# Kernel optimization log

Hardware: AMD Instinct MI355X
Metric: run time of the kernel (lower is better)

The kernel has to match this reference:

```python
import jax, jax.numpy as jnp
import numpy as np

B, T_D, T_P = 64, 256, 1024
DRUG_DIM, PROT_DIM, D = 128, 128, 128
MAX_LEN = 1024
NEG = -1e9


def _linear_params(k, out_d, in_d):
    k1, k2 = jax.random.split(k)
    lim = 1.0 / np.sqrt(in_d)
    W = jax.random.uniform(k1, (out_d, in_d), minval=-lim, maxval=lim, dtype=jnp.float32)
    b = jax.random.uniform(k2, (out_d,), minval=-lim, maxval=lim, dtype=jnp.float32)
    return W, b


def setup_inputs() -> dict:
    key = jax.random.key(0)
    ks = jax.random.split(key, 13)
    inp = {
        'smiles_embeddings': jax.random.normal(ks[0], (B, T_D, DRUG_DIM), dtype=jnp.float32),
        'protein_embeddings': jax.random.normal(ks[1], (B, T_P, PROT_DIM), dtype=jnp.float32),
        'smiles_mask': jax.random.randint(ks[2], (B, T_D), 0, 2, dtype=jnp.int32),
        'protein_mask': jax.random.randint(ks[3], (B, T_P), 0, 2, dtype=jnp.int32),
        # torch inits pos_bias to zeros; small random values make the test nontrivial
        'pos_bias': 0.02 * jax.random.normal(ks[4], (MAX_LEN, MAX_LEN), dtype=jnp.float32),
    }
    names = [('Wqd', 'bqd', DRUG_DIM), ('Wkp', 'bkp', PROT_DIM), ('Wvp', 'bvp', PROT_DIM),
             ('Wqp', 'bqp', PROT_DIM), ('Wkd', 'bkd', DRUG_DIM), ('Wvd', 'bvd', DRUG_DIM),
             ('Wpd', 'bpd', D), ('Wpp', 'bpp', D)]
    for i, (wn, bn, in_d) in enumerate(names):
        W, b = _linear_params(ks[5 + i], D, in_d)
        inp[wn] = W
        inp[bn] = b
    return inp


def _lin(x, W, b):
    return x @ W.T + b


def _aft(q, k, v, pb_masked, Wp, bp):
    # q: [B,Ti,D]; k,v: [B,Tj,D]; pb_masked: [B,Ti,Tj]
    max_k = k.max(axis=1, keepdims=True)              # per (b,d) over seq j
    max_pb = pb_masked.max(axis=2, keepdims=True)     # per (b,i) over j
    exp_k = jnp.exp(k - max_k)                        # [B,Tj,D]
    exp_pb = jnp.exp(pb_masked - max_pb)              # [B,Ti,Tj]
    num = jnp.einsum('bij,bjd->bid', exp_pb, exp_k * v)
    den = jnp.einsum('bij,bjd->bid', exp_pb, exp_k)
    y = jax.nn.sigmoid(q) * num / den
    return _lin(y, Wp, bp)


def reference(smiles_embeddings, protein_embeddings, smiles_mask, protein_mask, pos_bias,
              Wqd, bqd, Wkp, bkp, Wvp, bvp, Wqp, bqp, Wkd, bkd, Wvd, bvd, Wpd, bpd, Wpp, bpp):
    Td = smiles_embeddings.shape[1]
    Tp = protein_embeddings.shape[1]
    combined = smiles_mask[:, :, None] * protein_mask[:, None, :]  # [B,Td,Tp]
    pb = pos_bias[:Td, :Tp][None]                                   # [1,Td,Tp]

    # drug queries attend over protein keys/values
    pb_d = jnp.where(combined == 0, NEG, pb)
    y_d = _aft(_lin(smiles_embeddings, Wqd, bqd),
               _lin(protein_embeddings, Wkp, bkp),
               _lin(protein_embeddings, Wvp, bvp), pb_d, Wpd, bpd)

    # protein queries attend over drug keys/values (transposed pos bias)
    pb_p = jnp.where(jnp.swapaxes(combined, 1, 2) == 0, NEG, jnp.swapaxes(pb, 1, 2))
    y_p = _aft(_lin(protein_embeddings, Wqp, bqp),
               _lin(smiles_embeddings, Wkd, bkd),
               _lin(smiles_embeddings, Wvd, bvd), pb_p, Wpp, bpp)

    y_d = jnp.where(smiles_mask[:, :, None] == 0, NEG, y_d).max(axis=1)   # [B,D]
    y_p = jnp.where(protein_mask[:, :, None] == 0, NEG, y_p).max(axis=1)  # [B,D]
    return y_d, y_p
```

## Files before the change

### kernel.cpp

```cpp
#include <hip/hip_runtime.h>
#include <cstdint>
#include <cstddef>

#define NEGV -1e9f

typedef __bf16 bf16x8 __attribute__((ext_vector_type(8)));
typedef float f32x4 __attribute__((ext_vector_type(4)));
typedef unsigned short us4 __attribute__((ext_vector_type(4)));
typedef unsigned short us8 __attribute__((ext_vector_type(8)));

__device__ __forceinline__ unsigned short f2bf(float f) {
  unsigned int u = __float_as_uint(f);
  u += 0x7fffu + ((u >> 16) & 1u);
  return (unsigned short)(u >> 16);
}
__device__ __forceinline__ float bf2f(unsigned short u) {
  return __uint_as_float(((unsigned)u) << 16);
}

__device__ __forceinline__ void gld16(const void* g, void* l) {
  __builtin_amdgcn_global_load_lds(
      (const __attribute__((address_space(1))) unsigned int*)g,
      (__attribute__((address_space(3))) unsigned int*)l, 16, 0, 0);
}

__global__ void wcvt_kernel(const float* __restrict__ w0, const float* __restrict__ w1,
                            const float* __restrict__ w2, const float* __restrict__ w3,
                            const float* __restrict__ w4, const float* __restrict__ w5,
                            const float* __restrict__ w6, const float* __restrict__ w7,
                            unsigned short* __restrict__ dst) {
  const float* Ws[8] = {w0, w1, w2, w3, w4, w5, w6, w7};
  const float* src = Ws[blockIdx.y];
  int idx = blockIdx.x * 256 + threadIdx.x;
  float4 v = *(const float4*)&src[(size_t)idx * 4];
  us4 p;
  p.x = f2bf(v.x); p.y = f2bf(v.y); p.z = f2bf(v.z); p.w = f2bf(v.w);
  *(us4*)&dst[(size_t)blockIdx.y * 16384 + (size_t)idx * 4] = p;
}

__global__ void epb_kernel(const float* __restrict__ pb,
                           unsigned short* __restrict__ epb,
                           unsigned short* __restrict__ epbT) {
  __shared__ unsigned short t[32][33];
  const int j0 = (blockIdx.x & 31) * 32, i0 = (blockIdx.x >> 5) * 32;
  const int tx = threadIdx.x & 31, ty = threadIdx.x >> 5;
#pragma unroll
  for (int r = 0; r < 4; ++r) {
    int i = i0 + ty + r * 8;
    unsigned short u = f2bf(__expf(pb[(size_t)i * 1024 + j0 + tx]));
    epb[(size_t)i * 1024 + j0 + tx] = u;
    t[ty + r * 8][tx] = u;
  }
  __syncthreads();
#pragma unroll
  for (int r = 0; r < 4; ++r)
    epbT[(size_t)(j0 + ty + r * 8) * 256 + i0 + tx] = t[tx][ty + r * 8];
}

template <int T>
__global__ __launch_bounds__(256) void proj3(
    const float* __restrict__ X, const int* __restrict__ mask,
    const unsigned short* __restrict__ Wq, const float* __restrict__ bq,
    const unsigned short* __restrict__ Wk, const float* __restrict__ bk_,
    const unsigned short* __restrict__ Wv, const float* __restrict__ bv,
    unsigned short* __restrict__ sigQ, unsigned short* __restrict__ eKT,
    unsigned short* __restrict__ eKVT) {
  __shared__ unsigned short smem[2 * 128 * 72];
  unsigned short* xL = smem;
  const int tid = threadIdx.x;
  const int g0 = blockIdx.x * 64;
  const int b = g0 / T;
  const int tl0 = g0 - b * T;

#pragma unroll
  for (int r = 0; r < 8; ++r) {
    int i4 = tid + 256 * r;
    int t = i4 >> 5, k4 = (i4 & 31) * 4;
    float4 v = *(const float4*)&X[(size_t)(g0 + t) * 128 + k4];
    us4 p;
    p.x = f2bf(v.x); p.y = f2bf(v.y); p.z = f2bf(v.z); p.w = f2bf(v.w);
    *(us4*)&xL[t * 136 + k4] = p;
  }
  __syncthreads();

  const int lane = tid & 63, wave = tid >> 6;
  const int lo = lane & 15, hi = lane >> 4;
  const int d0 = wave * 32;

  f32x4 aQ[4][2], aK[4][2], aV[4][2];
#pragma unroll
  for (int a = 0; a < 4; ++a)
#pragma unroll
    for (int s = 0; s < 2; ++s)
#pragma unroll
      for (int r = 0; r < 4; ++r) { aQ[a][s][r] = 0.f; aK[a][s][r] = 0.f; aV[a][s][r] = 0.f; }

#pragma unroll
  for (int kt = 0; kt < 128; kt += 32) {
    bf16x8 bQ[2], bK[2], bV[2];
#pragma unroll
    for (int s = 0; s < 2; ++s) {
      size_t roff = (size_t)(d0 + s * 16 + lo) * 128 + kt + hi * 8;
      bQ[s] = *(const bf16x8*)&Wq[roff];
      bK[s] = *(const bf16x8*)&Wk[roff];
      bV[s] = *(const bf16x8*)&Wv[roff];
    }
#pragma unroll
    for (int a = 0; a < 4; ++a) {
      bf16x8 af = *(const bf16x8*)&xL[(a * 16 + lo) * 136 + kt + hi * 8];
#pragma unroll
      for (int s = 0; s < 2; ++s) {
        aQ[a][s] = __builtin_amdgcn_mfma_f32_16x16x32_bf16(af, bQ[s], aQ[a][s], 0, 0, 0);
        aK[a][s] = __builtin_amdgcn_mfma_f32_16x16x32_bf16(af, bK[s], aK[a][s], 0, 0, 0);
        aV[a][s] = __builtin_amdgcn_mfma_f32_16x16x32_bf16(af, bV[s], aV[a][s], 0, 0, 0);
      }
    }
  }

#pragma unroll
  for (int s = 0; s < 2; ++s) {
    int d = d0 + s * 16 + lo;
    float bb = bq[d];
#pragma unroll
    for (int a = 0; a < 4; ++a)
#pragma unroll
      for (int r = 0; r < 4; ++r) {
        int t = g0 + a * 16 + hi * 4 + r;
        float q = aQ[a][s][r] + bb;
        sigQ[(size_t)t * 128 + d] = f2bf(1.f / (1.f + __expf(-q)));
      }
  }

  __syncthreads();
  unsigned short* ekL = smem;
  unsigned short* ekvL = smem + 9216;
#pragma unroll
  for (int s = 0; s < 2; ++s) {
    int d = d0 + s * 16 + lo;
    float bbk = bk_[d], bbv = bv[d];
#pragma unroll
    for (int a = 0; a < 4; ++a)
#pragma unroll
      for (int r = 0; r < 4; ++r) {
        int tl = a * 16 + hi * 4 + r;
        int mk = mask[g0 + tl];
        float ek = mk ? __expf(aK[a][s][r] + bbk) : 0.f;
        float ekv = ek * (aV[a][s][r] + bbv);
        ekL[d * 72 + tl] = f2bf(ek);
        ekvL[d * 72 + tl] = f2bf(ekv);
      }
  }
  __syncthreads();
#pragma unroll
  for (int r = 0; r < 8; ++r) {
    int q = tid + 256 * r;
    int arr = q >> 10, qq = q & 1023;
    int d = qq >> 3, c = qq & 7;
    us8 v = *(const us8*)&smem[arr * 9216 + d * 72 + c * 8];
    unsigned short* dst = arr ? eKVT : eKT;
    *(us8*)&dst[((size_t)b * 128 + d) * T + tl0 + c * 8] = v;
  }
}

__global__ __launch_bounds__(256, 2) void aft_all(
    const unsigned short* __restrict__ epb, const unsigned short* __restrict__ epbT,
    const unsigned short* __restrict__ eKTd, const unsigned short* __restrict__ eKVTd,
    const unsigned short* __restrict__ eKTp, const unsigned short* __restrict__ eKVTp,
    const unsigned short* __restrict__ sigQd, const unsigned short* __restrict__ sigQp,
    const int* __restrict__ smask, const int* __restrict__ pmask,
    const unsigned short* __restrict__ Wpd, const float* __restrict__ bpd,
    const unsigned short* __restrict__ Wpp, const float* __restrict__ bpp,
    unsigned int* __restrict__ outEnc) {
  __shared__ unsigned short smem[17408];
  unsigned short* bkL = smem;
  unsigned short* bvL = smem + 8192;

  const int blk = blockIdx.x;
  const unsigned short *Ap, *KT, *VT, *SQ, *Wp;
  const float* bp;
  const int* msk;
  unsigned int* oEnc;
  int b, i0, TJ, Ti, astr;
  if (blk < 128) {
    b = blk >> 1; i0 = (blk & 1) * 128; TJ = 1024; Ti = 256;
    Ap = epb; astr = 1024; KT = eKTp; VT = eKVTp; SQ = sigQd;
    Wp = Wpd; bp = bpd; msk = smask + b * 256 + i0; oEnc = outEnc;
  } else {
    int k = blk - 128;
    b = k >> 3; i0 = (k & 7) * 128; TJ = 256; Ti = 1024;
    Ap = epbT; astr = 256; KT = eKTd; VT = eKVTd; SQ = sigQp;
    Wp = Wpp; bp = bpp; msk = pmask + b * 1024 + i0; oEnc = outEnc + 8192;
  }

  const int tid = threadIdx.x, lane = tid & 63, w = tid >> 6;
  const int lo = lane & 15, hi = lane >> 4;
  const int wi = (w >> 1) * 64, wd = (w & 1) * 64;
  const unsigned short* KTb = KT + (size_t)b * 128 * TJ;
  const unsigned short* VTb = VT + (size_t)b * 128 * TJ;
  const int slotbase = w * 256;

  f32x4 aN[4][4], aD[4][4];
#pragma unroll
  for (int a = 0; a < 4; ++a)
#pragma unroll
    for (int n = 0; n < 4; ++n)
#pragma unroll
      for (int r = 0; r < 4; ++r) { aN[a][n][r] = 0.f; aD[a][n][r] = 0.f; }

  for (int jt = 0; jt < TJ; jt += 64) {
    __syncthreads();
#pragma unroll
    for (int it = 0; it < 4; ++it) {
      int slot = slotbase + it * 64 + lane;
      int r = slot >> 3, sc = slot & 7;
      int cg = sc ^ (r & 7);
      size_t goff = (size_t)r * TJ + jt + cg * 8;
      gld16(KTb + goff, &bkL[(slotbase + it * 64) * 8]);
      gld16(VTb + goff, &bvL[(slotbase + it * 64) * 8]);
    }
    bf16x8 af[4][2];
#pragma unroll
    for (int a = 0; a < 4; ++a)
#pragma unroll
      for (int kt = 0; kt < 2; ++kt)
        af[a][kt] = *(const bf16x8*)
            &Ap[(size_t)(i0 + wi + a * 16 + lo) * astr + jt + kt * 32 + hi * 8];
    __syncthreads();
#pragma unroll
    for (int kt = 0; kt < 2; ++kt) {
      bf16x8 bk[4], bv[4];
#pragma unroll
      for (int n = 0; n < 4; ++n) {
        int row = wd + n * 16 + lo;
        int sc = ((kt * 4 + hi) ^ (row & 7)) * 8;
        bk[n] = *(const bf16x8*)&bkL[row * 64 + sc];
        bv[n] = *(const bf16x8*)&bvL[row * 64 + sc];
      }
#pragma unroll
      for (int a = 0; a < 4; ++a)
#pragma unroll
        for (int n = 0; n < 4; ++n) {
          aN[a][n] = __builtin_amdgcn_mfma_f32_16x16x32_bf16(af[a][kt], bv[n], aN[a][n], 0, 0, 0);
          aD[a][n] = __builtin_amdgcn_mfma_f32_16x16x32_bf16(af[a][kt], bk[n], aD[a][n], 0, 0, 0);
        }
    }
  }

  __syncthreads();
  unsigned short* yL = smem;
#pragma unroll
  for (int a = 0; a < 4; ++a)
#pragma unroll
    for (int n = 0; n < 4; ++n) {
      int iL = wi + a * 16 + hi * 4;
      int d = wd + n * 16 + lo;
#pragma unroll
      for (int r = 0; r < 4; ++r) {
        size_t off = ((size_t)b * Ti + i0 + iL + r) * 128 + d;
        float s = bf2f(SQ[off]);
        float y = s * __fdividef(aN[a][n][r], aD[a][n][r]);
        yL[(iL + r) * 136 + d] = f2bf(y);
      }
    }
  __syncthreads();

  f32x4 aZ[4][4];
#pragma unroll
  for (int a = 0; a < 4; ++a)
#pragma unroll
    for (int n = 0; n < 4; ++n)
#pragma unroll
      for (int r = 0; r < 4; ++r) aZ[a][n][r] = 0.f;

#pragma unroll
  for (int kt = 0; kt < 128; kt += 32) {
    bf16x8 bw[4];
#pragma unroll
    for (int n = 0; n < 4; ++n)
      bw[n] = *(const bf16x8*)&Wp[(size_t)(wd + n * 16 + lo) * 128 + kt + hi * 8];
#pragma unroll
    for (int a = 0; a < 4; ++a) {
      bf16x8 af = *(const bf16x8*)&yL[(wi + a * 16 + lo) * 136 + kt + hi * 8];
#pragma unroll
      for (int n = 0; n < 4; ++n)
        aZ[a][n] = __builtin_amdgcn_mfma_f32_16x16x32_bf16(af, bw[n], aZ[a][n], 0, 0, 0);
    }
  }

#pragma unroll
  for (int n = 0; n < 4; ++n) {
    int d = wd + n * 16 + lo;
    float bb = bp[d];
    float m = NEGV;
#pragma unroll
    for (int a = 0; a < 4; ++a)
#pragma unroll
      for (int r = 0; r < 4; ++r) {
        int iL = wi + a * 16 + hi * 4 + r;
        float z = aZ[a][n][r] + bb;
        m = msk[iL] ? fmaxf(m, z) : m;
      }
    m = fmaxf(m, __shfl_xor(m, 16, 64));
    m = fmaxf(m, __shfl_xor(m, 32, 64));
    if (hi == 0) {
      unsigned bits = __float_as_uint(m);
      unsigned key = (bits & 0x80000000u) ? ~bits : (bits | 0x80000000u);
      atomicMax(&oEnc[b * 128 + d], key);
    }
  }
}

__global__ void out_init(unsigned int* o) {
  o[blockIdx.x * 256 + threadIdx.x] = 0u;
}
__global__ void out_decode(unsigned int* o) {
  int i = blockIdx.x * 256 + threadIdx.x;
  unsigned k = o[i];
  unsigned bits = (k & 0x80000000u) ? (k ^ 0x80000000u) : ~k;
  ((float*)o)[i] = __uint_as_float(bits);
}

extern "C" void kernel_launch(void* const* d_in, const int* in_sizes, int n_in,
                              void* d_out, int out_size, void* d_ws, size_t ws_size,
                              hipStream_t stream) {
  const float* smiles = (const float*)d_in[0];
  const float* prot   = (const float*)d_in[1];
  const int* smask = (const int*)d_in[2];
  const int* pmask = (const int*)d_in[3];
  const float* pos_bias = (const float*)d_in[4];
  const float* Wqd = (const float*)d_in[5];  const float* bqd = (const float*)d_in[6];
  const float* Wkp = (const float*)d_in[7];  const float* bkp = (const float*)d_in[8];
  const float* Wvp = (const float*)d_in[9];  const float* bvp = (const float*)d_in[10];
  const float* Wqp = (const float*)d_in[11]; const float* bqp = (const float*)d_in[12];
  const float* Wkd = (const float*)d_in[13]; const float* bkd = (const float*)d_in[14];
  const float* Wvd = (const float*)d_in[15]; const float* bvd = (const float*)d_in[16];
  const float* Wpd = (const float*)d_in[17]; const float* bpd = (const float*)d_in[18];
  const float* Wpp = (const float*)d_in[19]; const float* bpp = (const float*)d_in[20];

  unsigned short* u = (unsigned short*)d_ws;
  unsigned short* eKTp  = u;
  unsigned short* eKVTp = eKTp + 8388608;
  unsigned short* eKTd  = eKVTp + 8388608;
  unsigned short* eKVTd = eKTd + 2097152;
  unsigned short* sigQd = eKVTd + 2097152;
  unsigned short* sigQp = sigQd + 2097152;
  unsigned short* epb_  = sigQp + 8388608;
  unsigned short* epbT_ = epb_ + 262144;
  unsigned short* Wbf   = epbT_ + 262144;

  dim3 blk(256);

  out_init<<<64, blk, 0, stream>>>((unsigned int*)d_out);
  wcvt_kernel<<<dim3(16, 8), blk, 0, stream>>>(Wqd, Wkd, Wvd, Wqp, Wkp, Wvp, Wpd, Wpp, Wbf);
  epb_kernel<<<256, blk, 0, stream>>>(pos_bias, epb_, epbT_);

  proj3<256><<<256, blk, 0, stream>>>(smiles, smask,
      Wbf + 0 * 16384, bqd, Wbf + 1 * 16384, bkd, Wbf + 2 * 16384, bvd,
      sigQd, eKTd, eKVTd);
  proj3<1024><<<1024, blk, 0, stream>>>(prot, pmask,
      Wbf + 3 * 16384, bqp, Wbf + 4 * 16384, bkp, Wbf + 5 * 16384, bvp,
      sigQp, eKTp, eKVTp);

  aft_all<<<640, blk, 0, stream>>>(epb_, epbT_, eKTd, eKVTd, eKTp, eKVTp,
                                   sigQd, sigQp, smask, pmask,
                                   Wbf + 6 * 16384, bpd, Wbf + 7 * 16384, bpp,
                                   (unsigned int*)d_out);

  out_decode<<<64, blk, 0, stream>>>((unsigned int*)d_out);
}
```

Baseline: 207.2 us.

## Merge prep and projection launches and double-buffer AFT K/V tiles

Folds output init, weight conversion and exp(pos_bias) into a single prep kernel, and merges the two projection launches into one grid, cutting launch count and tail gaps. In the AFT kernel, K/V tiles are now double-buffered in LDS (shared memory grows to 64 KB) and the next A fragments are prefetched into registers, with manual waitcnt/barrier so loads overlap the MFMA work. The block-to-(batch, row-tile) mapping is also reordered so batches are spread across the grid. The larger LDS footprint and extra registers may lower occupancy, and the hand-written vmcnt value must match the number of outstanding loads.

```diff
diff --git a/kernel.cpp b/kernel.cpp
--- a/kernel.cpp
+++ b/kernel.cpp
@@ -24,26 +24,34 @@
       (__attribute__((address_space(3))) unsigned int*)l, 16, 0, 0);
 }
 
-__global__ void wcvt_kernel(const float* __restrict__ w0, const float* __restrict__ w1,
+__global__ void prep_kernel(const float* __restrict__ w0, const float* __restrict__ w1,
                             const float* __restrict__ w2, const float* __restrict__ w3,
                             const float* __restrict__ w4, const float* __restrict__ w5,
                             const float* __restrict__ w6, const float* __restrict__ w7,
-                            unsigned short* __restrict__ dst) {
-  const float* Ws[8] = {w0, w1, w2, w3, w4, w5, w6, w7};
-  const float* src = Ws[blockIdx.y];
-  int idx = blockIdx.x * 256 + threadIdx.x;
-  float4 v = *(const float4*)&src[(size_t)idx * 4];
-  us4 p;
-  p.x = f2bf(v.x); p.y = f2bf(v.y); p.z = f2bf(v.z); p.w = f2bf(v.w);
-  *(us4*)&dst[(size_t)blockIdx.y * 16384 + (size_t)idx * 4] = p;
-}
-
-__global__ void epb_kernel(const float* __restrict__ pb,
-                           unsigned short* __restrict__ epb,
-                           unsigned short* __restrict__ epbT) {
+                            unsigned short* __restrict__ Wbf,
+                            const float* __restrict__ pb,
+                            unsigned short* __restrict__ epb,
+                            unsigned short* __restrict__ epbT,
+                            unsigned int* __restrict__ outEnc) {
   __shared__ unsigned short t[32][33];
-  const int j0 = (blockIdx.x & 31) * 32, i0 = (blockIdx.x >> 5) * 32;
-  const int tx = threadIdx.x & 31, ty = threadIdx.x >> 5;
+  const int blk = blockIdx.x, tid = threadIdx.x;
+  if (blk < 64) {
+    outEnc[blk * 256 + tid] = 0u;
+    return;
+  }
+  if (blk < 192) {
+    const float* Ws[8] = {w0, w1, w2, w3, w4, w5, w6, w7};
+    int idx = (blk - 64) * 256 + tid;
+    int mat = idx >> 12, off = idx & 4095;
+    float4 v = *(const float4*)&Ws[mat][(size_t)off * 4];
+    us4 p;
+    p.x = f2bf(v.x); p.y = f2bf(v.y); p.z = f2bf(v.z); p.w = f2bf(v.w);
+    *(us4*)&Wbf[(size_t)mat * 16384 + (size_t)off * 4] = p;
+    return;
+  }
+  const int bid = blk - 192;
+  const int j0 = (bid & 31) * 32, i0 = (bid >> 5) * 32;
+  const int tx = tid & 31, ty = tid >> 5;
 #pragma unroll
   for (int r = 0; r < 4; ++r) {
     int i = i0 + ty + r * 8;
@@ -57,18 +65,36 @@
     epbT[(size_t)(j0 + ty + r * 8) * 256 + i0 + tx] = t[tx][ty + r * 8];
 }
 
-template <int T>
-__global__ __launch_bounds__(256) void proj3(
-    const float* __restrict__ X, const int* __restrict__ mask,
-    const unsigned short* __restrict__ Wq, const float* __restrict__ bq,
-    const unsigned short* __restrict__ Wk, const float* __restrict__ bk_,
-    const unsigned short* __restrict__ Wv, const float* __restrict__ bv,
-    unsigned short* __restrict__ sigQ, unsigned short* __restrict__ eKT,
-    unsigned short* __restrict__ eKVT) {
+__global__ __launch_bounds__(256) void proj3_all(
+    const float* __restrict__ smiles, const float* __restrict__ prot,
+    const int* __restrict__ smask, const int* __restrict__ pmask,
+    const unsigned short* __restrict__ Wbf,
+    const float* __restrict__ bqd, const float* __restrict__ bkd, const float* __restrict__ bvd,
+    const float* __restrict__ bqp, const float* __restrict__ bkp, const float* __restrict__ bvp,
+    unsigned short* __restrict__ sigQd, unsigned short* __restrict__ eKTd,
+    unsigned short* __restrict__ eKVTd,
+    unsigned short* __restrict__ sigQp, unsigned short* __restrict__ eKTp,
+    unsigned short* __restrict__ eKVTp) {
   __shared__ unsigned short smem[2 * 128 * 72];
   unsigned short* xL = smem;
   const int tid = threadIdx.x;
-  const int g0 = blockIdx.x * 64;
+
+  const float* X; const int* mask;
+  const unsigned short *Wq, *Wk, *Wv;
+  const float *bq, *bk_, *bv;
+  unsigned short *sigQ, *eKT, *eKVT;
+  int T, g0;
+  if (blockIdx.x < 256) {
+    X = smiles; mask = smask; T = 256; g0 = blockIdx.x * 64;
+    Wq = Wbf; Wk = Wbf + 16384; Wv = Wbf + 32768;
+    bq = bqd; bk_ = bkd; bv = bvd;
+    sigQ = sigQd; eKT = eKTd; eKVT = eKVTd;
+  } else {
+    X = prot; mask = pmask; T = 1024; g0 = (blockIdx.x - 256) * 64;
+    Wq = Wbf + 3 * 16384; Wk = Wbf + 4 * 16384; Wv = Wbf + 5 * 16384;
+    bq = bqp; bk_ = bkp; bv = bvp;
+    sigQ = sigQp; eKT = eKTp; eKVT = eKVTp;
+  }
   const int b = g0 / T;
   const int tl0 = g0 - b * T;
 
@@ -168,12 +194,10 @@
     const unsigned short* __restrict__ eKTp, const unsigned short* __restrict__ eKVTp,
     const unsigned short* __restrict__ sigQd, const unsigned short* __restrict__ sigQp,
     const int* __restrict__ smask, const int* __restrict__ pmask,
-    const unsigned short* __restrict__ Wpd, const float* __restrict__ bpd,
-    const unsigned short* __restrict__ Wpp, const float* __restrict__ bpp,
+    const unsigned short* __restrict__ Wbf,
+    const float* __restrict__ bpd, const float* __restrict__ bpp,
     unsigned int* __restrict__ outEnc) {
-  __shared__ unsigned short smem[17408];
-  unsigned short* bkL = smem;
-  unsigned short* bvL = smem + 8192;
+  __shared__ unsigned short smem[32768];
 
   const int blk = blockIdx.x;
   const unsigned short *Ap, *KT, *VT, *SQ, *Wp;
@@ -182,14 +206,14 @@
   unsigned int* oEnc;
   int b, i0, TJ, Ti, astr;
   if (blk < 128) {
-    b = blk >> 1; i0 = (blk & 1) * 128; TJ = 1024; Ti = 256;
+    b = blk & 63; i0 = (blk >> 6) * 128; TJ = 1024; Ti = 256;
     Ap = epb; astr = 1024; KT = eKTp; VT = eKVTp; SQ = sigQd;
-    Wp = Wpd; bp = bpd; msk = smask + b * 256 + i0; oEnc = outEnc;
+    Wp = Wbf + 6 * 16384; bp = bpd; msk = smask + b * 256 + i0; oEnc = outEnc;
   } else {
     int k = blk - 128;
-    b = k >> 3; i0 = (k & 7) * 128; TJ = 256; Ti = 1024;
+    b = k & 63; i0 = (k >> 6) * 128; TJ = 256; Ti = 1024;
     Ap = epbT; astr = 256; KT = eKTd; VT = eKVTd; SQ = sigQp;
-    Wp = Wpp; bp = bpp; msk = pmask + b * 1024 + i0; oEnc = outEnc + 8192;
+    Wp = Wbf + 7 * 16384; bp = bpp; msk = pmask + b * 1024 + i0; oEnc = outEnc + 8192;
   }
 
   const int tid = threadIdx.x, lane = tid & 63, w = tid >> 6;
@@ -199,16 +223,9 @@
   const unsigned short* VTb = VT + (size_t)b * 128 * TJ;
   const int slotbase = w * 256;
 
-  f32x4 aN[4][4], aD[4][4];
-#pragma unroll
-  for (int a = 0; a < 4; ++a)
-#pragma unroll
-    for (int n = 0; n < 4; ++n)
-#pragma unroll
-      for (int r = 0; r < 4; ++r) { aN[a][n][r] = 0.f; aD[a][n][r] = 0.f; }
-
-  for (int jt = 0; jt < TJ; jt += 64) {
-    __syncthreads();
+  auto stage = [&](int jt, int p) {
+    unsigned short* bkL = smem + p * 16384;
+    unsigned short* bvL = bkL + 8192;
 #pragma unroll
     for (int it = 0; it < 4; ++it) {
       int slot = slotbase + it * 64 + lane;
@@ -218,14 +235,40 @@
       gld16(KTb + goff, &bkL[(slotbase + it * 64) * 8]);
       gld16(VTb + goff, &bvL[(slotbase + it * 64) * 8]);
     }
-    bf16x8 af[4][2];
+  };
+
+  f32x4 aN[4][4], aD[4][4];
+#pragma unroll
+  for (int a = 0; a < 4; ++a)
+#pragma unroll
+    for (int n = 0; n < 4; ++n)
+#pragma unroll
+      for (int r = 0; r < 4; ++r) { aN[a][n][r] = 0.f; aD[a][n][r] = 0.f; }
+
+  stage(0, 0);
+  bf16x8 af_cur[4][2];
+#pragma unroll
+  for (int a = 0; a < 4; ++a)
+#pragma unroll
+    for (int kt = 0; kt < 2; ++kt)
+      af_cur[a][kt] = *(const bf16x8*)
+          &Ap[(size_t)(i0 + wi + a * 16 + lo) * astr + kt * 32 + hi * 8];
+
+  int p = 0;
+  for (int jt = 0; jt < TJ; jt += 64) {
+    const int jn = (jt + 64 < TJ) ? jt + 64 : jt;
+    stage(jn, p ^ 1);
+    bf16x8 af_nxt[4][2];
 #pragma unroll
     for (int a = 0; a < 4; ++a)
 #pragma unroll
       for (int kt = 0; kt < 2; ++kt)
-        af[a][kt] = *(const bf16x8*)
-            &Ap[(size_t)(i0 + wi + a * 16 + lo) * astr + jt + kt * 32 + hi * 8];
-    __syncthreads();
+        af_nxt[a][kt] = *(const bf16x8*)
+            &Ap[(size_t)(i0 + wi + a * 16 + lo) * astr + jn + kt * 32 + hi * 8];
+    asm volatile("s_waitcnt vmcnt(16)\ns_barrier" ::: "memory");
+
+    const unsigned short* bkL = smem + p * 16384;
+    const unsigned short* bvL = bkL + 8192;
 #pragma unroll
     for (int kt = 0; kt < 2; ++kt) {
       bf16x8 bk[4], bv[4];
@@ -240,10 +283,17 @@
       for (int a = 0; a < 4; ++a)
 #pragma unroll
         for (int n = 0; n < 4; ++n) {
-          aN[a][n] = __builtin_amdgcn_mfma_f32_16x16x32_bf16(af[a][kt], bv[n], aN[a][n], 0, 0, 0);
-          aD[a][n] = __builtin_amdgcn_mfma_f32_16x16x32_bf16(af[a][kt], bk[n], aD[a][n], 0, 0, 0);
+          aN[a][n] = __builtin_amdgcn_mfma_f32_16x16x32_bf16(af_cur[a][kt], bv[n], aN[a][n], 0, 0, 0);
+          aD[a][n] = __builtin_amdgcn_mfma_f32_16x16x32_bf16(af_cur[a][kt], bk[n], aD[a][n], 0, 0, 0);
         }
     }
+    asm volatile("s_waitcnt lgkmcnt(0)\ns_barrier" ::: "memory");
+#pragma unroll
+    for (int a = 0; a < 4; ++a)
+#pragma unroll
+      for (int kt = 0; kt < 2; ++kt)
+        af_cur[a][kt] = af_nxt[a][kt];
+    p ^= 1;
   }
 
   __syncthreads();
@@ -310,9 +360,6 @@
   }
 }
 
-__global__ void out_init(unsigned int* o) {
-  o[blockIdx.x * 256 + threadIdx.x] = 0u;
-}
 __global__ void out_decode(unsigned int* o) {
   int i = blockIdx.x * 256 + threadIdx.x;
   unsigned k = o[i];
@@ -350,21 +397,17 @@
 
   dim3 blk(256);
 
-  out_init<<<64, blk, 0, stream>>>((unsigned int*)d_out);
-  wcvt_kernel<<<dim3(16, 8), blk, 0, stream>>>(Wqd, Wkd, Wvd, Wqp, Wkp, Wvp, Wpd, Wpp, Wbf);
-  epb_kernel<<<256, blk, 0, stream>>>(pos_bias, epb_, epbT_);
-
-  proj3<256><<<256, blk, 0, stream>>>(smiles, smask,
-      Wbf + 0 * 16384, bqd, Wbf + 1 * 16384, bkd, Wbf + 2 * 16384, bvd,
-      sigQd, eKTd, eKVTd);
-  proj3<1024><<<1024, blk, 0, stream>>>(prot, pmask,
-      Wbf + 3 * 16384, bqp, Wbf + 4 * 16384, bkp, Wbf + 5 * 16384, bvp,
-      sigQp, eKTp, eKVTp);
+  prep_kernel<<<448, blk, 0, stream>>>(Wqd, Wkd, Wvd, Wqp, Wkp, Wvp, Wpd, Wpp,
+                                       Wbf, pos_bias, epb_, epbT_,
+                                       (unsigned int*)d_out);
+
+  proj3_all<<<1280, blk, 0, stream>>>(smiles, prot, smask, pmask, Wbf,
+                                      bqd, bkd, bvd, bqp, bkp, bvp,
+                                      sigQd, eKTd, eKVTd, sigQp, eKTp, eKVTp);
 
   aft_all<<<640, blk, 0, stream>>>(epb_, epbT_, eKTd, eKVTd, eKTp, eKVTp,
-                                   sigQd, sigQp, smask, pmask,
-                                   Wbf + 6 * 16384, bpd, Wbf + 7 * 16384, bpp,
-                                   (unsigned int*)d_out);
+                                   sigQd, sigQp, smask, pmask, Wbf,
+                                   bpd, bpp, (unsigned int*)d_out);
 
   out_decode<<<64, blk, 0, stream>>>((unsigned int*)d_out);
 }
```

New measurement: 196.5 us. -5.2%, faster.
